# Performance work log

Hardware: AMD Instinct MI355X
Metric: run time of the kernel (lower is better)

The kernel has to match this reference:

```python
import jax, jax.numpy as jnp
import numpy as np

N, D, NUM_CLASSES = 8192, 128, 1000


def setup_inputs() -> dict:
    key = jax.random.key(0)
    ka, kb, kt = jax.random.split(key, 3)
    fa = jax.random.normal(ka, (N, D), dtype=jnp.float32)
    fb = jax.random.normal(kb, (N, D), dtype=jnp.float32)
    # L2-normalize as in standard contrastive setups (CLIP-style)
    fa = fa / jnp.linalg.norm(fa, axis=-1, keepdims=True)
    fb = fb / jnp.linalg.norm(fb, axis=-1, keepdims=True)
    targets = jax.random.randint(kt, (N,), 0, NUM_CLASSES, dtype=jnp.int64 if jax.config.jax_enable_x64 else jnp.int32)
    T = jnp.array([100.0], dtype=jnp.float32)  # logit scale
    return {
        "T": T,
        "local_features_a": fa,
        "local_features_b": fb,
        "global_targets": targets,
        "training": 1,
    }


def reference(T, local_features_a, local_features_b, global_targets, training):
    # world_size = 1: local features ARE the global features; the chunked
    # online-softmax reduction in the original is mathematically identical
    # to a stable logsumexp over the full logits row (max is detached, so
    # gradients also match).
    eq = (global_targets[:, None] == global_targets[None, :]).astype(jnp.float32)  # [N, N] positive mask
    target_sum = jnp.sum(eq, axis=-1)  # [N]

    def one_direction(fa, fb):
        logits = T * (fa @ fb.T)  # [N, N]
        weighted = -jnp.sum(eq * logits, axis=-1)            # sum of -logits over positives
        lse = jax.nn.logsumexp(logits, axis=-1)              # online-softmax global reduction
        per_row = weighted / target_sum + lse                # [N]
        return jnp.mean(per_row)

    loss_i = one_direction(local_features_a, local_features_b)
    loss_t = one_direction(local_features_b, local_features_a)
    return (loss_i + loss_t) / 2.0
```

## Files before the change

### kernel.cpp

```cpp
#include <hip/hip_runtime.h>
#include <hip/hip_bf16.h>

#define CN 8192
#define CD 128
#define NCLS 1000
#define MAXC 256

typedef __attribute__((ext_vector_type(8))) short bf16x8;
typedef __attribute__((ext_vector_type(4))) float f32x4;

#define WS_B_OFF     0x200000u
#define WS_CNT_OFF   0x400000u
#define WS_EXTRA_OFF 0x401000u
#define WS_ROWE_OFF  0x402000u
#define WS_COLE_OFF  0x40A000u
#define WS_BKT_OFF   0x412000u
#define WS_ROWP_OFF  0x490000u
#define WS_COLP_OFF  0x890000u
#define WS_FAST_BYTES 0xA90000u
#define WS_ZERO_BYTES 0x12000u

__device__ inline unsigned short f2bf(float f) {
    unsigned int u = __float_as_uint(f);
    return (unsigned short)((u + 0x7FFFu + ((u >> 16) & 1u)) >> 16);
}

__global__ void convert_kernel(const float* __restrict__ fa, const float* __restrict__ fb,
                               unsigned short* __restrict__ Abf, unsigned short* __restrict__ Bbf,
                               const int* __restrict__ tgt,
                               int* __restrict__ cnt, unsigned short* __restrict__ bucket) {
    int gid = blockIdx.x * 256 + threadIdx.x;
    int i = gid * 4;
    const float* src = blockIdx.y == 0 ? fa : fb;
    unsigned short* dst = blockIdx.y == 0 ? Abf : Bbf;
    float4 v = *reinterpret_cast<const float4*>(src + i);
    ushort4 o;
    o.x = f2bf(v.x); o.y = f2bf(v.y); o.z = f2bf(v.z); o.w = f2bf(v.w);
    *reinterpret_cast<ushort4*>(dst + i) = o;

    if (blockIdx.y == 0 && (gid & 31) == 0) {
        int row = gid >> 5;
        int t = tgt[row];
        int slot = atomicAdd(&cnt[t], 1);
        if (slot < MAXC) bucket[t * MAXC + slot] = (unsigned short)row;
    }
}

__global__ __launch_bounds__(64) void classsum_kernel(
    const float* __restrict__ Tptr,
    const float* __restrict__ fa, const float* __restrict__ fb,
    const int* __restrict__ cnt, const unsigned short* __restrict__ bucket,
    float* __restrict__ extra) {
    const int c = blockIdx.x;
    const int lane = threadIdx.x;
    const int n = cnt[c];
    const int m = n < MAXC ? n : MAXC;
    const float* src = lane < 32 ? fa : fb;
    const int d = (lane & 31) * 4;
    float ax = 0.f, ay = 0.f, az = 0.f, aw = 0.f;
    for (int s = 0; s < m; ++s) {
        int row = bucket[c * MAXC + s];
        float4 v = *reinterpret_cast<const float4*>(src + (size_t)row * CD + d);
        ax += v.x; ay += v.y; az += v.z; aw += v.w;
    }
    float bx_ = __shfl_xor(ax, 32), by_ = __shfl_xor(ay, 32);
    float bz_ = __shfl_xor(az, 32), bw_ = __shfl_xor(aw, 32);
    float p = ax * bx_ + ay * by_ + az * bz_ + aw * bw_;
    #pragma unroll
    for (int off = 1; off < 32; off <<= 1) p += __shfl_xor(p, off);
    if (lane == 0) extra[c] = n > 0 ? (-2.0f * Tptr[0] * p / (float)n) : 0.f;
}

__global__ __launch_bounds__(256) void tile_kernel(
    const float* __restrict__ Tptr,
    const unsigned short* __restrict__ Abf,
    const unsigned short* __restrict__ Bbf,
    float* __restrict__ rowE, float* __restrict__ colE,
    float* __restrict__ rowPart, float* __restrict__ colPart,
    int store_mode)
{
    __shared__ __align__(16) unsigned short sA[128 * 128];
    __shared__ __align__(16) unsigned short sB[2][64 * 128];
    __shared__ float colRed[2][4][64];

    const int tid   = threadIdx.x;
    const int bx    = blockIdx.x;
    const int by    = blockIdx.y;
    const int brow  = by * 128;
    const int cbase = bx * 1024;
    const float T   = Tptr[0];
    const float Tl2 = T * 1.44269504088896340736f;

    #pragma unroll
    for (int it = 0; it < 8; ++it) {
        int idx = it * 256 + tid;
        int r = idx >> 4, q = idx & 15;
        const unsigned short* src = Abf + (size_t)(brow + r) * CD + ((q ^ (r & 7)) * 8);
        __builtin_amdgcn_global_load_lds((const __attribute__((address_space(1))) void*)src,
                                         (__attribute__((address_space(3))) void*)&sA[idx * 8],
                                         16, 0, 0);
    }
    #pragma unroll
    for (int it = 0; it < 4; ++it) {
        int idx = it * 256 + tid;
        int r = idx >> 4, q = idx & 15;
        const unsigned short* src = Bbf + (size_t)(cbase + r) * CD + ((q ^ (r & 7)) * 8);
        __builtin_amdgcn_global_load_lds((const __attribute__((address_space(1))) void*)src,
                                         (__attribute__((address_space(3))) void*)&sB[0][idx * 8],
                                         16, 0, 0);
    }
    __syncthreads();

    const int lane = tid & 63;
    const int w    = tid >> 6;
    const int colg = lane & 15;
    const int rowg = lane >> 4;

    float rE[2][4] = {{0.f, 0.f, 0.f, 0.f}, {0.f, 0.f, 0.f, 0.f}};

    for (int ct = 0; ct < 16; ++ct) {
        const int cur = ct & 1;
        if (ct < 15) {
            int bcolN = cbase + (ct + 1) * 64;
            #pragma unroll
            for (int it = 0; it < 4; ++it) {
                int idx = it * 256 + tid;
                int r = idx >> 4, q = idx & 15;
                const unsigned short* src = Bbf + (size_t)(bcolN + r) * CD + ((q ^ (r & 7)) * 8);
                __builtin_amdgcn_global_load_lds((const __attribute__((address_space(1))) void*)src,
                                                 (__attribute__((address_space(3))) void*)&sB[cur ^ 1][idx * 8],
                                                 16, 0, 0);
            }
        }

        f32x4 acc[2][4];
        #pragma unroll
        for (int m = 0; m < 2; ++m)
            #pragma unroll
            for (int n = 0; n < 4; ++n)
                acc[m][n] = (f32x4){0.f, 0.f, 0.f, 0.f};

        #pragma unroll
        for (int kk = 0; kk < 4; ++kk) {
            bf16x8 af[2], bfr[4];
            #pragma unroll
            for (int m = 0; m < 2; ++m) {
                int r = w * 32 + m * 16 + colg;
                int slot = (kk * 4 + rowg) ^ (r & 7);
                af[m] = *reinterpret_cast<const bf16x8*>(&sA[r * 128 + slot * 8]);
            }
            #pragma unroll
            for (int n = 0; n < 4; ++n) {
                int r = n * 16 + colg;
                int slot = (kk * 4 + rowg) ^ (r & 7);
                bfr[n] = *reinterpret_cast<const bf16x8*>(&sB[cur][r * 128 + slot * 8]);
            }
            #pragma unroll
            for (int m = 0; m < 2; ++m)
                #pragma unroll
                for (int n = 0; n < 4; ++n)
                    acc[m][n] = __builtin_amdgcn_mfma_f32_16x16x32_bf16(af[m], bfr[n], acc[m][n], 0, 0, 0);
        }

        float cE[4] = {0.f, 0.f, 0.f, 0.f};
        #pragma unroll
        for (int m = 0; m < 2; ++m)
            #pragma unroll
            for (int n = 0; n < 4; ++n)
                #pragma unroll
                for (int j = 0; j < 4; ++j) {
                    float e = exp2f(__builtin_fmaf(acc[m][n][j], Tl2, -Tl2));
                    rE[m][j] += e;
                    cE[n]    += e;
                }

        #pragma unroll
        for (int n = 0; n < 4; ++n) {
            float e = cE[n];
            e += __shfl_xor(e, 16);
            e += __shfl_xor(e, 32);
            if (rowg == 0) colRed[cur][w][n * 16 + colg] = e;
        }
        __syncthreads();
        if (tid < 64) {
            float s = colRed[cur][0][tid] + colRed[cur][1][tid]
                    + colRed[cur][2][tid] + colRed[cur][3][tid];
            int col = cbase + ct * 64 + tid;
            if (store_mode) colPart[(size_t)by * CN + col] = s;
            else            atomicAdd(&colE[col], s);
        }
    }

    #pragma unroll
    for (int m = 0; m < 2; ++m)
        #pragma unroll
        for (int j = 0; j < 4; ++j) {
            float e = rE[m][j];
            #pragma unroll
            for (int off = 1; off < 16; off <<= 1) e += __shfl_xor(e, off);
            if (colg == 0) {
                int row = brow + w * 32 + m * 16 + rowg * 4 + j;
                if (store_mode) rowPart[(size_t)bx * CN + row] = e;
                else            atomicAdd(&rowE[row], e);
            }
        }
}

__global__ __launch_bounds__(256) void finalize_kernel(
    const float* __restrict__ Tptr,
    const float* __restrict__ rowE, const float* __restrict__ colE,
    const float* __restrict__ rowPart, const float* __restrict__ colPart,
    const float* __restrict__ extra,
    float* __restrict__ out, int store_mode)
{
    __shared__ float red[4];
    const int tid = threadIdx.x;
    int i = blockIdx.x * 256 + tid;
    const float T = Tptr[0];
    float v = 0.f;
    if (i < CN) {
        float se;
        if (store_mode) {
            se = 0.f;
            #pragma unroll
            for (int p = 0; p < 8; ++p) se += rowPart[(size_t)p * CN + i];
        } else se = rowE[i];
        v = T + logf(se);
    } else if (i < 2 * CN) {
        int c = i - CN;
        float se;
        if (store_mode) {
            se = 0.f;
            #pragma unroll 4
            for (int p = 0; p < 64; ++p) se += colPart[(size_t)p * CN + c];
        } else se = colE[c];
        v = T + logf(se);
    } else if (i < 2 * CN + NCLS) {
        v = extra[i - 2 * CN];
    }
    #pragma unroll
    for (int off = 1; off < 64; off <<= 1) v += __shfl_xor(v, off);
    if ((tid & 63) == 0) red[tid >> 6] = v;
    __syncthreads();
    if (tid == 0) {
        float tot = red[0] + red[1] + red[2] + red[3];
        atomicAdd(out, tot * (1.0f / (2.0f * (float)CN)));
    }
}

extern "C" void kernel_launch(void* const* d_in, const int* in_sizes, int n_in,
                              void* d_out, int out_size, void* d_ws, size_t ws_size,
                              hipStream_t stream) {
    const float* T  = (const float*)d_in[0];
    const float* fa = (const float*)d_in[1];
    const float* fb = (const float*)d_in[2];
    const int* tgt  = (const int*)d_in[3];
    float* out      = (float*)d_out;

    char* ws = (char*)d_ws;
    unsigned short* Abf = (unsigned short*)ws;
    unsigned short* Bbf = (unsigned short*)(ws + WS_B_OFF);
    int*   cnt    = (int*)(ws + WS_CNT_OFF);
    float* extra  = (float*)(ws + WS_EXTRA_OFF);
    float* rowE   = (float*)(ws + WS_ROWE_OFF);
    float* colE   = (float*)(ws + WS_COLE_OFF);
    unsigned short* bucket = (unsigned short*)(ws + WS_BKT_OFF);
    float* rowPart = (float*)(ws + WS_ROWP_OFF);
    float* colPart = (float*)(ws + WS_COLP_OFF);

    const int store_mode = (ws_size >= WS_FAST_BYTES) ? 1 : 0;

    hipMemsetAsync(out, 0, sizeof(float), stream);
    hipMemsetAsync(ws + WS_CNT_OFF, 0, WS_ZERO_BYTES, stream);

    convert_kernel<<<dim3(CN * CD / (256 * 4), 2), 256, 0, stream>>>(fa, fb, Abf, Bbf, tgt, cnt, bucket);
    classsum_kernel<<<NCLS, 64, 0, stream>>>(T, fa, fb, cnt, bucket, extra);

    dim3 grid(8, 64);
    tile_kernel<<<grid, 256, 0, stream>>>(T, Abf, Bbf, rowE, colE, rowPart, colPart, store_mode);

    finalize_kernel<<<(2 * CN + NCLS + 255) / 256, 256, 0, stream>>>(
        T, rowE, colE, rowPart, colPart, extra, out, store_mode);
}
```

Baseline: 131.4 us.

## Merge class-sum into tile kernel and finalize with last-block write

Folds the per-class feature-sum work into the main tile kernel as 250 extra blocks, each handling four classes with one wave per class. This removes a separate kernel launch and lets the class sums run alongside the tiled GEMM/logsumexp blocks. The finalize kernel now accumulates into a workspace counter and the last block writes the output, which removes the memset of the output buffer. The cost is that class-sum blocks take the same LDS allocation as tile blocks, which may cut occupancy, and the final result now depends on a correct threadfence and counter handshake.

```diff
diff --git a/kernel.cpp b/kernel.cpp
--- a/kernel.cpp
+++ b/kernel.cpp
@@ -5,6 +5,8 @@
 #define CD 128
 #define NCLS 1000
 #define MAXC 256
+#define CLS_BLOCKS 250
+#define TILE_BLOCKS 512
 
 typedef __attribute__((ext_vector_type(8))) short bf16x8;
 typedef __attribute__((ext_vector_type(4))) float f32x4;
@@ -14,11 +16,13 @@
 #define WS_EXTRA_OFF 0x401000u
 #define WS_ROWE_OFF  0x402000u
 #define WS_COLE_OFF  0x40A000u
-#define WS_BKT_OFF   0x412000u
+#define WS_ACC_OFF   0x412000u
+#define WS_DONE_OFF  0x412004u
+#define WS_BKT_OFF   0x413000u
 #define WS_ROWP_OFF  0x490000u
 #define WS_COLP_OFF  0x890000u
 #define WS_FAST_BYTES 0xA90000u
-#define WS_ZERO_BYTES 0x12000u
+#define WS_ZERO_BYTES 0x12100u
 
 __device__ inline unsigned short f2bf(float f) {
     unsigned int u = __float_as_uint(f);
@@ -46,35 +50,13 @@
     }
 }
 
-__global__ __launch_bounds__(64) void classsum_kernel(
-    const float* __restrict__ Tptr,
-    const float* __restrict__ fa, const float* __restrict__ fb,
-    const int* __restrict__ cnt, const unsigned short* __restrict__ bucket,
-    float* __restrict__ extra) {
-    const int c = blockIdx.x;
-    const int lane = threadIdx.x;
-    const int n = cnt[c];
-    const int m = n < MAXC ? n : MAXC;
-    const float* src = lane < 32 ? fa : fb;
-    const int d = (lane & 31) * 4;
-    float ax = 0.f, ay = 0.f, az = 0.f, aw = 0.f;
-    for (int s = 0; s < m; ++s) {
-        int row = bucket[c * MAXC + s];
-        float4 v = *reinterpret_cast<const float4*>(src + (size_t)row * CD + d);
-        ax += v.x; ay += v.y; az += v.z; aw += v.w;
-    }
-    float bx_ = __shfl_xor(ax, 32), by_ = __shfl_xor(ay, 32);
-    float bz_ = __shfl_xor(az, 32), bw_ = __shfl_xor(aw, 32);
-    float p = ax * bx_ + ay * by_ + az * bz_ + aw * bw_;
-    #pragma unroll
-    for (int off = 1; off < 32; off <<= 1) p += __shfl_xor(p, off);
-    if (lane == 0) extra[c] = n > 0 ? (-2.0f * Tptr[0] * p / (float)n) : 0.f;
-}
-
-__global__ __launch_bounds__(256) void tile_kernel(
+__global__ __launch_bounds__(256) void mega_kernel(
     const float* __restrict__ Tptr,
     const unsigned short* __restrict__ Abf,
     const unsigned short* __restrict__ Bbf,
+    const float* __restrict__ fa, const float* __restrict__ fb,
+    const int* __restrict__ cnt, const unsigned short* __restrict__ bucket,
+    float* __restrict__ extra,
     float* __restrict__ rowE, float* __restrict__ colE,
     float* __restrict__ rowPart, float* __restrict__ colPart,
     int store_mode)
@@ -83,9 +65,35 @@
     __shared__ __align__(16) unsigned short sB[2][64 * 128];
     __shared__ float colRed[2][4][64];
 
-    const int tid   = threadIdx.x;
-    const int bx    = blockIdx.x;
-    const int by    = blockIdx.y;
+    const int bid  = blockIdx.x;
+    const int tid  = threadIdx.x;
+    const int lane = tid & 63;
+    const int w    = tid >> 6;
+
+    if (bid < CLS_BLOCKS) {
+        const int c = bid * 4 + w;
+        const int n = cnt[c];
+        const int m = n < MAXC ? n : MAXC;
+        const float* src = lane < 32 ? fa : fb;
+        const int d = (lane & 31) * 4;
+        float ax = 0.f, ay = 0.f, az = 0.f, aw = 0.f;
+        for (int s = 0; s < m; ++s) {
+            int row = bucket[c * MAXC + s];
+            float4 v = *reinterpret_cast<const float4*>(src + (size_t)row * CD + d);
+            ax += v.x; ay += v.y; az += v.z; aw += v.w;
+        }
+        float bx_ = __shfl_xor(ax, 32), by_ = __shfl_xor(ay, 32);
+        float bz_ = __shfl_xor(az, 32), bw_ = __shfl_xor(aw, 32);
+        float p = ax * bx_ + ay * by_ + az * bz_ + aw * bw_;
+        #pragma unroll
+        for (int off = 1; off < 32; off <<= 1) p += __shfl_xor(p, off);
+        if (lane == 0) extra[c] = n > 0 ? (-2.0f * Tptr[0] * p / (float)n) : 0.f;
+        return;
+    }
+
+    const int tb    = bid - CLS_BLOCKS;
+    const int bx    = tb & 7;
+    const int by    = tb >> 3;
     const int brow  = by * 128;
     const int cbase = bx * 1024;
     const float T   = Tptr[0];
@@ -111,8 +119,6 @@
     }
     __syncthreads();
 
-    const int lane = tid & 63;
-    const int w    = tid >> 6;
     const int colg = lane & 15;
     const int rowg = lane >> 4;
 
@@ -211,6 +217,7 @@
     const float* __restrict__ rowE, const float* __restrict__ colE,
     const float* __restrict__ rowPart, const float* __restrict__ colPart,
     const float* __restrict__ extra,
+    float* __restrict__ wsAcc, unsigned int* __restrict__ wsDone,
     float* __restrict__ out, int store_mode)
 {
     __shared__ float red[4];
@@ -244,7 +251,13 @@
     __syncthreads();
     if (tid == 0) {
         float tot = red[0] + red[1] + red[2] + red[3];
-        atomicAdd(out, tot * (1.0f / (2.0f * (float)CN)));
+        atomicAdd(wsAcc, tot);
+        __threadfence();
+        unsigned int old = atomicAdd(wsDone, 1u);
+        if (old == gridDim.x - 1) {
+            float total = atomicAdd(wsAcc, 0.0f);
+            out[0] = total * (1.0f / (2.0f * (float)CN));
+        }
     }
 }
 
@@ -264,21 +277,22 @@
     float* extra  = (float*)(ws + WS_EXTRA_OFF);
     float* rowE   = (float*)(ws + WS_ROWE_OFF);
     float* colE   = (float*)(ws + WS_COLE_OFF);
+    float* wsAcc  = (float*)(ws + WS_ACC_OFF);
+    unsigned int* wsDone = (unsigned int*)(ws + WS_DONE_OFF);
     unsigned short* bucket = (unsigned short*)(ws + WS_BKT_OFF);
     float* rowPart = (float*)(ws + WS_ROWP_OFF);
     float* colPart = (float*)(ws + WS_COLP_OFF);
 
     const int store_mode = (ws_size >= WS_FAST_BYTES) ? 1 : 0;
 
-    hipMemsetAsync(out, 0, sizeof(float), stream);
     hipMemsetAsync(ws + WS_CNT_OFF, 0, WS_ZERO_BYTES, stream);
 
     convert_kernel<<<dim3(CN * CD / (256 * 4), 2), 256, 0, stream>>>(fa, fb, Abf, Bbf, tgt, cnt, bucket);
-    classsum_kernel<<<NCLS, 64, 0, stream>>>(T, fa, fb, cnt, bucket, extra);
-
-    dim3 grid(8, 64);
-    tile_kernel<<<grid, 256, 0, stream>>>(T, Abf, Bbf, rowE, colE, rowPart, colPart, store_mode);
+
+    mega_kernel<<<CLS_BLOCKS + TILE_BLOCKS, 256, 0, stream>>>(
+        T, Abf, Bbf, fa, fb, cnt, bucket, extra,
+        rowE, colE, rowPart, colPart, store_mode);
 
     finalize_kernel<<<(2 * CN + NCLS + 255) / 256, 256, 0, stream>>>(
-        T, rowE, colE, rowPart, colPart, extra, out, store_mode);
-}
+        T, rowE, colE, rowPart, colPart, extra, wsAcc, wsDone, out, store_mode);
+}
```

Measured after the change: 126.1 us. 4.0% less time.
